# Kernel tuning notes

Hardware: AMD Instinct MI355X
Metric: run time of the kernel (lower is better)

Reference implementation:

```python
import jax, jax.numpy as jnp
import numpy as np

D = 512
HEADS, DIM_HEAD, LANDMARKS, PINV_ITERS = 8, 64, 256, 6
CONV_K = 33  # residual depthwise conv kernel over sequence dim


def _ln(x, g, b, eps=1e-5):
    mu = x.mean(-1, keepdims=True)
    var = ((x - mu) ** 2).mean(-1, keepdims=True)
    return (x - mu) / jnp.sqrt(var + eps) * g + b


def _moe(x, gw, gb, f1w, f1b, l1g, l1b, f2w, f2b, l2g, l2b, k):
    # Dense grouped-expert evaluation (same math as per-token dispatch in torch source).
    scores = x @ gw + gb                               # [B,N,E]
    topk_s, topk_i = jax.lax.top_k(scores, k)          # [B,N,k]
    h = jnp.einsum('bnd,edh->benh', x, f1w) + f1b[None, :, None, :]
    h = jax.nn.relu(_ln(h, l1g[None, :, None, :], l1b[None, :, None, :]))
    o = jnp.einsum('benh,ehd->bend', h, f2w) + f2b[None, :, None, :]
    o = _ln(o, l2g[None, :, None, :], l2b[None, :, None, :])  # [B,E,N,D]
    o = jnp.take_along_axis(jnp.swapaxes(o, 1, 2), topk_i[..., None], axis=2)  # [B,N,k,D]
    w = jax.nn.softmax(topk_s, axis=-1)[..., None]
    return (w * o).sum(axis=2) + x


def _pinv(x, iters):
    # Moore-Penrose iterative pseudoinverse (lucidrains nystrom-attention)
    col = jnp.abs(x).sum(-1).max()
    row = jnp.abs(x).sum(-2).max()
    z = jnp.swapaxes(x, -1, -2) / (col * row)
    I = jnp.eye(x.shape[-1], dtype=x.dtype)
    for _ in range(iters):
        xz = x @ z
        z = 0.25 * z @ (13 * I - xz @ (15 * I - xz @ (7 * I - xz)))
    return z


def _nystrom(x, qkv_w, out_w, out_b, conv_w):
    b, n, _ = x.shape
    m, h, dh = LANDMARKS, HEADS, DIM_HEAD
    pad = (m - n % m) % m
    x = jnp.pad(x, ((0, 0), (pad, 0), (0, 0)))  # pad at FRONT, as in source
    npd = n + pad
    qkv = x @ qkv_w                              # [b, npd, 3*h*dh]
    q, k, v = [t.reshape(b, npd, h, dh).transpose(0, 2, 1, 3) for t in jnp.split(qkv, 3, axis=-1)]
    q = q * dh ** -0.5
    l = npd // m
    q_l = q.reshape(b, h, m, l, dh).mean(3)      # landmark means
    k_l = k.reshape(b, h, m, l, dh).mean(3)
    attn1 = jax.nn.softmax(jnp.einsum('bhid,bhjd->bhij', q, k_l), -1)    # [b,h,npd,m]
    attn2 = jax.nn.softmax(jnp.einsum('bhid,bhjd->bhij', q_l, k_l), -1)  # [b,h,m,m]
    attn3 = jax.nn.softmax(jnp.einsum('bhid,bhjd->bhij', q_l, k), -1)    # [b,h,m,npd]
    out = (attn1 @ _pinv(attn2, PINV_ITERS)) @ (attn3 @ v)               # [b,h,npd,dh]
    res = jax.lax.conv_general_dilated(
        v, conv_w, (1, 1), [(CONV_K // 2, CONV_K // 2), (0, 0)],
        dimension_numbers=('NCHW', 'OIHW', 'NCHW'), feature_group_count=h)
    out = out + res
    out = out.transpose(0, 2, 1, 3).reshape(b, npd, h * dh)
    out = out @ out_w + out_b
    return out[:, -n:]


def setup_inputs() -> dict:
    key = jax.random.key(0)
    ks = iter(jax.random.split(key, 64))
    def rn(shape, s=0.02):
        return jax.random.normal(next(ks), shape, jnp.float32) * s
    inp = {'features': jax.random.normal(next(ks), (4, 6000, D), jnp.float32)}
    inp['cls_token'] = rn((1, 1, D), 1e-6)
    def moe_params(pfx, E):
        inp[pfx + '_gate_w'] = rn((D, E)); inp[pfx + '_gate_b'] = jnp.zeros((E,), jnp.float32)
        inp[pfx + '_fc1_w'] = rn((E, D, D)); inp[pfx + '_fc1_b'] = jnp.zeros((E, D), jnp.float32)
        inp[pfx + '_ln1_g'] = jnp.ones((E, D), jnp.float32); inp[pfx + '_ln1_b'] = jnp.zeros((E, D), jnp.float32)
        inp[pfx + '_fc2_w'] = rn((E, D, D)); inp[pfx + '_fc2_b'] = jnp.zeros((E, D), jnp.float32)
        inp[pfx + '_ln2_g'] = jnp.ones((E, D), jnp.float32); inp[pfx + '_ln2_b'] = jnp.zeros((E, D), jnp.float32)
    moe_params('moe1', 2)
    moe_params('moe2', 4)
    def layer_params(pfx):
        inp[pfx + '_norm_g'] = jnp.ones((D,), jnp.float32); inp[pfx + '_norm_b'] = jnp.zeros((D,), jnp.float32)
        inp[pfx + '_qkv_w'] = rn((D, 3 * HEADS * DIM_HEAD))
        inp[pfx + '_out_w'] = rn((HEADS * DIM_HEAD, D)); inp[pfx + '_out_b'] = jnp.zeros((D,), jnp.float32)
        inp[pfx + '_conv_w'] = rn((HEADS, 1, CONV_K, 1))
    layer_params('l1')
    layer_params('l2')
    return inp


def reference(features, cls_token,
              moe1_gate_w, moe1_gate_b, moe1_fc1_w, moe1_fc1_b, moe1_ln1_g, moe1_ln1_b, moe1_fc2_w, moe1_fc2_b, moe1_ln2_g, moe1_ln2_b,
              moe2_gate_w, moe2_gate_b, moe2_fc1_w, moe2_fc1_b, moe2_ln1_g, moe2_ln1_b, moe2_fc2_w, moe2_fc2_b, moe2_ln2_g, moe2_ln2_b,
              l1_norm_g, l1_norm_b, l1_qkv_w, l1_out_w, l1_out_b, l1_conv_w,
              l2_norm_g, l2_norm_b, l2_qkv_w, l2_out_w, l2_out_b, l2_conv_w):
    B, N, _ = features.shape
    _H = int(np.ceil(np.sqrt(N)))
    add = _H * _H - N
    h = jnp.concatenate([features, features[:, :add]], axis=1)      # square pad by wrap
    h = jnp.concatenate([jnp.broadcast_to(cls_token, (B, 1, D)), h], axis=1)
    h = _moe(h, moe1_gate_w, moe1_gate_b, moe1_fc1_w, moe1_fc1_b, moe1_ln1_g, moe1_ln1_b, moe1_fc2_w, moe1_fc2_b, moe1_ln2_g, moe1_ln2_b, k=1)
    h = h + _nystrom(_ln(h, l1_norm_g, l1_norm_b), l1_qkv_w, l1_out_w, l1_out_b, l1_conv_w)
    h = _moe(h, moe2_gate_w, moe2_gate_b, moe2_fc1_w, moe2_fc1_b, moe2_ln1_g, moe2_ln1_b, moe2_fc2_w, moe2_fc2_b, moe2_ln2_g, moe2_ln2_b, k=2)
    h = h + _nystrom(_ln(h, l2_norm_g, l2_norm_b), l2_qkv_w, l2_out_w, l2_out_b, l2_conv_w)
    return (h[:, 0], h[:, 1:])
```

## Files before the change

kernel.cpp:

```cpp
#include <hip/hip_runtime.h>
#include <hip/hip_bf16.h>

constexpr int BATCH = 4;
constexpr int NTOK  = 6085;
constexpr int BN_TOK = BATCH * NTOK;
constexpr int NPD   = 6144;
constexpr int RPAD  = BATCH * NPD;
constexpr int DMODEL = 512;
constexpr int NH = 8, DH = 64;
constexpr int NBH = BATCH * NH;
constexpr int LGRP = NPD / 256;
constexpr int PAD_FRONT = 59;
constexpr int CONVK = 33;
constexpr int NCH = 8;

typedef __attribute__((ext_vector_type(8))) short short8v;
typedef __attribute__((ext_vector_type(4))) float f32x4;

__device__ __forceinline__ unsigned short f2bf(float f) {
  unsigned u = __float_as_uint(f);
  u += 0x7FFF + ((u >> 16) & 1);
  return (unsigned short)(u >> 16);
}
__device__ __forceinline__ float bf2f(unsigned short h) {
  return __uint_as_float((unsigned)h << 16);
}


__global__ void k_build_h(const float* __restrict__ feat, const float* __restrict__ cls,
                          float* __restrict__ H) {
  size_t total = (size_t)BN_TOK * DMODEL;
  for (size_t idx = (size_t)blockIdx.x * blockDim.x + threadIdx.x; idx < total;
       idx += (size_t)gridDim.x * blockDim.x) {
    int d = (int)(idx & 511);
    size_t tok = idx >> 9;
    int b = (int)(tok / NTOK), n = (int)(tok % NTOK);
    float v;
    if (n == 0) v = cls[d];
    else {
      int i = n - 1; if (i >= 6000) i -= 6000;
      v = feat[((size_t)b * 6000 + i) * DMODEL + d];
    }
    H[idx] = v;
  }
}

__global__ void k_diag_fill(float* __restrict__ out, size_t n, float val) {
  for (size_t i = (size_t)blockIdx.x * blockDim.x + threadIdx.x; i < n;
       i += (size_t)gridDim.x * blockDim.x)
    out[i] = val;
}

__global__ __launch_bounds__(256) void k_wconv(const float* __restrict__ W, int ldb,
    unsigned short* __restrict__ hi, unsigned short* __restrict__ lo) {
  __shared__ unsigned short Th[64][80], Tl[64][80];
  int bk = blockIdx.y * 64, bn = blockIdx.x * 64;
  int t = threadIdx.x;
  int kr = t >> 2, cq = (t & 3) * 16;
  const float* src = W + (size_t)(bk + kr) * ldb + bn + cq;
  #pragma unroll
  for (int q = 0; q < 4; ++q) {
    float4 v = *(const float4*)(src + q * 4);
    float vs[4] = {v.x, v.y, v.z, v.w};
    #pragma unroll
    for (int e = 0; e < 4; ++e) {
      int n = cq + q * 4 + e;
      unsigned short h = f2bf(vs[e]);
      Th[n][kr] = h;
      Tl[n][kr] = f2bf(vs[e] - bf2f(h));
    }
  }
  __syncthreads();
  int nr = t >> 2, kq = (t & 3) * 16;
  size_t o = (size_t)(bn + nr) * 512 + bk + kq;
  *(short8v*)&hi[o]     = *(const short8v*)&Th[nr][kq];
  *(short8v*)&hi[o + 8] = *(const short8v*)&Th[nr][kq + 8];
  *(short8v*)&lo[o]     = *(const short8v*)&Tl[nr][kq];
  *(short8v*)&lo[o + 8] = *(const short8v*)&Tl[nr][kq + 8];
}

__global__ __launch_bounds__(256) void k_gemm_mfma(const float* __restrict__ A,
    const unsigned short* __restrict__ BtH, const unsigned short* __restrict__ BtL,
    const float* __restrict__ bias, float* __restrict__ C,
    int M, int lda, int ldc, float alpha, int omode, unsigned short* __restrict__ Clo)
{
  __shared__ unsigned short AsH[128][40], AsL[128][40];
  __shared__ unsigned short BsH[128][40], BsL[128][40];
  int bm = blockIdx.y * 128, bn = blockIdx.x * 128;
  int tid = threadIdx.x;
  int wave = tid >> 6, lane = tid & 63;
  int mo = (wave >> 1) * 64, no = (wave & 1) * 64;
  int r16 = lane & 15, g = lane >> 4;
  f32x4 acc[4][4] = {};
  int srow = tid >> 1, shalf = (tid & 1) * 16;
  const float* aptr = A + (size_t)(bm + srow) * lda + shalf;
  bool avalid = (bm + srow) < M;
  const unsigned short* bhptr = BtH + (size_t)(bn + srow) * 512 + shalf;
  const unsigned short* blptr = BtL + (size_t)(bn + srow) * 512 + shalf;
  for (int k0 = 0; k0 < 512; k0 += 32) {
    unsigned short h8[16], l8[16];
    #pragma unroll
    for (int q = 0; q < 4; ++q) {
      float4 v = avalid ? *(const float4*)(aptr + k0 + q * 4) : make_float4(0.f, 0.f, 0.f, 0.f);
      float vs[4] = {v.x, v.y, v.z, v.w};
      #pragma unroll
      for (int e = 0; e < 4; ++e) {
        unsigned short hh = f2bf(vs[e]);
        h8[q * 4 + e] = hh;
        l8[q * 4 + e] = f2bf(vs[e] - bf2f(hh));
      }
    }
    *(short8v*)&AsH[srow][shalf]     = *(short8v*)&h8[0];
    *(short8v*)&AsH[srow][shalf + 8] = *(short8v*)&h8[8];
    *(short8v*)&AsL[srow][shalf]     = *(short8v*)&l8[0];
    *(short8v*)&AsL[srow][shalf + 8] = *(short8v*)&l8[8];
    *(short8v*)&BsH[srow][shalf]     = *(const short8v*)(bhptr + k0);
    *(short8v*)&BsH[srow][shalf + 8] = *(const short8v*)(bhptr + k0 + 8);
    *(short8v*)&BsL[srow][shalf]     = *(const short8v*)(blptr + k0);
    *(short8v*)&BsL[srow][shalf + 8] = *(const short8v*)(blptr + k0 + 8);
    __syncthreads();
    short8v ah[4], al[4], bh[4], bl[4];
    #pragma unroll
    for (int mt = 0; mt < 4; ++mt) {
      ah[mt] = *(const short8v*)&AsH[mo + mt * 16 + r16][g * 8];
      al[mt] = *(const short8v*)&AsL[mo + mt * 16 + r16][g * 8];
    }
    #pragma unroll
    for (int nt = 0; nt < 4; ++nt) {
      bh[nt] = *(const short8v*)&BsH[no + nt * 16 + r16][g * 8];
      bl[nt] = *(const short8v*)&BsL[no + nt * 16 + r16][g * 8];
    }
    #pragma unroll
    for (int mt = 0; mt < 4; ++mt)
      #pragma unroll
      for (int nt = 0; nt < 4; ++nt) {
        acc[mt][nt] = __builtin_amdgcn_mfma_f32_16x16x32_bf16(ah[mt], bh[nt], acc[mt][nt], 0, 0, 0);
        acc[mt][nt] = __builtin_amdgcn_mfma_f32_16x16x32_bf16(ah[mt], bl[nt], acc[mt][nt], 0, 0, 0);
        acc[mt][nt] = __builtin_amdgcn_mfma_f32_16x16x32_bf16(al[mt], bh[nt], acc[mt][nt], 0, 0, 0);
      }
    __syncthreads();
  }
  #pragma unroll
  for (int mt = 0; mt < 4; ++mt)
    #pragma unroll
    for (int nt = 0; nt < 4; ++nt)
      #pragma unroll
      for (int j = 0; j < 4; ++j) {
        int gr = bm + mo + mt * 16 + g * 4 + j;
        int gc = bn + no + nt * 16 + r16;
        if (gr >= M) continue;
        float v = alpha * acc[mt][nt][j] + (bias ? bias[gc] : 0.f);
        if (omode == 0) {
          C[(size_t)gr * ldc + gc] = v;
        } else if (omode == 2) {
          int bb = gr / NPD, ii = gr % NPD;
          if (ii >= PAD_FRONT)
            C[((size_t)bb * NTOK + ii - PAD_FRONT) * 512 + gc] += v;
        } else if (omode == 3) {
          int bb = gr / NPD, ii = gr % NPD;
          int hh = gc >> 6, dd = gc & 63;
          C[(((size_t)bb * NH + hh) * NPD + ii) * 64 + dd] = v;
        } else {
          int bb = gr / NPD, ii = gr % NPD;
          int hh = gc >> 6, dd = gc & 63;
          size_t idx = (((size_t)bb * NH + hh) * NPD + ii) * 64 + dd;
          unsigned short hi = f2bf(v);
          ((unsigned short*)C)[idx] = hi;
          Clo[idx] = f2bf(v - bf2f(hi));
        }
      }
}

__global__ __launch_bounds__(256) void k_gemm_mfma2(const float* __restrict__ A,
    const float* __restrict__ Bt, float* __restrict__ C,
    float alpha, int omode, float cdiag, int premap)
{
  __shared__ unsigned short AsH[128][40], AsL[128][40];
  __shared__ unsigned short BsH[128][40], BsL[128][40];
  size_t zo = (size_t)blockIdx.z * 65536;
  int bm = blockIdx.y * 128, bn = blockIdx.x * 128;
  int tid = threadIdx.x;
  int wave = tid >> 6, lane = tid & 63;
  int mo = (wave >> 1) * 64, no = (wave & 1) * 64;
  int r16 = lane & 15, g = lane >> 4;
  f32x4 acc[4][4] = {};
  int srow = tid >> 1, shalf = (tid & 1) * 16;
  int grow = bm + srow;
  int gn = bn + srow;
  for (int k0 = 0; k0 < 256; k0 += 32) {
    unsigned short h8[16], l8[16];
    #pragma unroll
    for (int q = 0; q < 4; ++q) {
      float4 v = *(const float4*)&A[zo + (size_t)grow * 256 + k0 + shalf + q * 4];
      float vs[4] = {v.x, v.y, v.z, v.w};
      #pragma unroll
      for (int e = 0; e < 4; ++e) {
        float a = vs[e];
        if (premap) a = ((grow == (k0 + shalf + q * 4 + e)) ? 7.f : 0.f) - a;
        unsigned short hh = f2bf(a);
        h8[q * 4 + e] = hh;
        l8[q * 4 + e] = f2bf(a - bf2f(hh));
      }
    }
    *(short8v*)&AsH[srow][shalf]     = *(short8v*)&h8[0];
    *(short8v*)&AsH[srow][shalf + 8] = *(short8v*)&h8[8];
    *(short8v*)&AsL[srow][shalf]     = *(short8v*)&l8[0];
    *(short8v*)&AsL[srow][shalf + 8] = *(short8v*)&l8[8];
    #pragma unroll
    for (int q = 0; q < 4; ++q) {
      float4 v = *(const float4*)&Bt[zo + (size_t)gn * 256 + k0 + shalf + q * 4];
      float vs[4] = {v.x, v.y, v.z, v.w};
      #pragma unroll
      for (int e = 0; e < 4; ++e) {
        unsigned short hh = f2bf(vs[e]);
        h8[q * 4 + e] = hh;
        l8[q * 4 + e] = f2bf(vs[e] - bf2f(hh));
      }
    }
    *(short8v*)&BsH[srow][shalf]     = *(short8v*)&h8[0];
    *(short8v*)&BsH[srow][shalf + 8] = *(short8v*)&h8[8];
    *(short8v*)&BsL[srow][shalf]     = *(short8v*)&l8[0];
    *(short8v*)&BsL[srow][shalf + 8] = *(short8v*)&l8[8];
    __syncthreads();
    short8v ah[4], al[4], bh[4], bl[4];
    #pragma unroll
    for (int mt = 0; mt < 4; ++mt) {
      ah[mt] = *(const short8v*)&AsH[mo + mt * 16 + r16][g * 8];
      al[mt] = *(const short8v*)&AsL[mo + mt * 16 + r16][g * 8];
    }
    #pragma unroll
    for (int nt = 0; nt < 4; ++nt) {
      bh[nt] = *(const short8v*)&BsH[no + nt * 16 + r16][g * 8];
      bl[nt] = *(const short8v*)&BsL[no + nt * 16 + r16][g * 8];
    }
    #pragma unroll
    for (int mt = 0; mt < 4; ++mt)
      #pragma unroll
      for (int nt = 0; nt < 4; ++nt) {
        acc[mt][nt] = __builtin_amdgcn_mfma_f32_16x16x32_bf16(ah[mt], bh[nt], acc[mt][nt], 0, 0, 0);
        acc[mt][nt] = __builtin_amdgcn_mfma_f32_16x16x32_bf16(ah[mt], bl[nt], acc[mt][nt], 0, 0, 0);
        acc[mt][nt] = __builtin_amdgcn_mfma_f32_16x16x32_bf16(al[mt], bh[nt], acc[mt][nt], 0, 0, 0);
      }
    __syncthreads();
  }
  #pragma unroll
  for (int mt = 0; mt < 4; ++mt)
    #pragma unroll
    for (int nt = 0; nt < 4; ++nt)
      #pragma unroll
      for (int j = 0; j < 4; ++j) {
        int gr = bm + mo + mt * 16 + g * 4 + j;
        int gc = bn + no + nt * 16 + r16;
        float v;
        if (omode == 5) v = ((gr == gc) ? cdiag : 0.f) - acc[mt][nt][j];
        else            v = alpha * acc[mt][nt][j];
        C[zo + (size_t)gr * 256 + gc] = v;
      }
}

__global__ __launch_bounds__(256) void k_tpose(const float* __restrict__ in,
                                               float* __restrict__ out) {
  __shared__ float Ts[64][65];
  int bx = blockIdx.x * 64, by = blockIdx.y * 64;
  size_t zo = (size_t)blockIdx.z * 65536;
  int t = threadIdx.x;
  int r = t >> 4, c4 = (t & 15) * 4;
  #pragma unroll
  for (int u = 0; u < 4; ++u) {
    float4 v = *(const float4*)&in[zo + (size_t)(by + r + u * 16) * 256 + bx + c4];
    Ts[r + u * 16][c4 + 0] = v.x; Ts[r + u * 16][c4 + 1] = v.y;
    Ts[r + u * 16][c4 + 2] = v.z; Ts[r + u * 16][c4 + 3] = v.w;
  }
  __syncthreads();
  #pragma unroll
// ... 90 lines not shown
__global__ void k_gate(const float* __restrict__ X, const float* __restrict__ gw,
                       const float* __restrict__ gb, float* __restrict__ WT, int E, int k) {
  int tok = blockIdx.x; int lane = threadIdx.x;
  const float* x = X + (size_t)tok * DMODEL;
  float s[4] = {0.f, 0.f, 0.f, 0.f};
  for (int d = lane; d < DMODEL; d += 64) {
    float xv = x[d];
    for (int e = 0; e < E; ++e) s[e] += xv * gw[(size_t)d * E + e];
  }
  #pragma unroll
  for (int off = 32; off; off >>= 1) {
    #pragma unroll
    for (int e = 0; e < 4; ++e) s[e] += __shfl_down(s[e], off);
  }
  if (lane == 0) {
    for (int e = 0; e < E; ++e) s[e] += gb[e];
    float w[4] = {0.f, 0.f, 0.f, 0.f};
    int i1 = 0;
    for (int e = 1; e < E; ++e) if (s[e] > s[i1]) i1 = e;
    if (k == 1) {
      w[i1] = 1.f;
    } else {
      int i2 = -1;
      for (int e = 0; e < E; ++e) { if (e == i1) continue; if (i2 < 0 || s[e] > s[i2]) i2 = e; }
      float e2 = expf(s[i2] - s[i1]);
      float zz = 1.f + e2;
      w[i1] = 1.f / zz; w[i2] = e2 / zz;
    }
    #pragma unroll
    for (int e = 0; e < 4; ++e) WT[(size_t)tok * 4 + e] = w[e];
  }
}

__device__ __forceinline__ void wave_ln_stats(const float* x, int lane, float& mu, float& rstd) {
  float s = 0.f, q = 0.f;
  #pragma unroll
  for (int j = 0; j < 8; ++j) { float v = x[lane + 64 * j]; s += v; q += v * v; }
  #pragma unroll
  for (int off = 32; off; off >>= 1) { s += __shfl_xor(s, off); q += __shfl_xor(q, off); }
  mu = s * (1.f / 512.f);
  float var = q * (1.f / 512.f) - mu * mu;
  rstd = rsqrtf(var + 1e-5f);
}

__global__ void k_ln_relu(float* __restrict__ T, const float* __restrict__ g,
                          const float* __restrict__ b) {
  int row = blockIdx.x; int lane = threadIdx.x;
  float* x = T + (size_t)row * 512;
  float mu, rstd; wave_ln_stats(x, lane, mu, rstd);
  #pragma unroll
  for (int j = 0; j < 8; ++j) {
    int d = lane + 64 * j;
    float v = (x[d] - mu) * rstd * g[d] + b[d];
    x[d] = fmaxf(v, 0.f);
  }
}

__global__ void k_ln_waccum(const float* __restrict__ T, float* __restrict__ H,
                            const float* __restrict__ g, const float* __restrict__ b,
                            const float* __restrict__ WT, int e) {
  int row = blockIdx.x;
  float w = WT[(size_t)row * 4 + e];
  if (w == 0.f) return;
  int lane = threadIdx.x;
  const float* x = T + (size_t)row * 512;
  float mu, rstd; wave_ln_stats(x, lane, mu, rstd);
  float* h = H + (size_t)row * 512;
  #pragma unroll
  for (int j = 0; j < 8; ++j) {
    int d = lane + 64 * j;
    h[d] += w * ((x[d] - mu) * rstd * g[d] + b[d]);
  }
}

__global__ void k_ln_pad(const float* __restrict__ H, float* __restrict__ XLn,
                         const float* __restrict__ g, const float* __restrict__ b) {
  int row = blockIdx.x; int lane = threadIdx.x;
  int bb = row / NPD, i = row % NPD;
  float* y = XLn + (size_t)row * 512;
  if (i < PAD_FRONT) {
    #pragma unroll
    for (int j = 0; j < 8; ++j) y[lane + 64 * j] = 0.f;
    return;
  }
  const float* x = H + ((size_t)bb * NTOK + (i - PAD_FRONT)) * 512;
  float mu, rstd; wave_ln_stats(x, lane, mu, rstd);
  #pragma unroll
  for (int j = 0; j < 8; ++j) {
    int d = lane + 64 * j;
    y[d] = (x[d] - mu) * rstd * g[d] + b[d];
  }
}

__global__ void k_xmean(const float* __restrict__ XLn, float* __restrict__ Xm) {
  int z = blockIdx.x;
  int c = threadIdx.x;
  int b = z >> 8, jm = z & 255;
  const float* base = XLn + ((size_t)b * NPD + jm * LGRP) * 512 + c;
  float s = 0.f;
  #pragma unroll
  for (int t = 0; t < LGRP; ++t) s += base[(size_t)t * 512];
  Xm[(size_t)z * 512 + c] = s * (1.f / LGRP);
}

__global__ __launch_bounds__(256) void k_attn2(const float* __restrict__ QL,
                                               const float* __restrict__ KL,
                                               float* __restrict__ A2) {
  int z = blockIdx.x; int bh = z >> 8, j = z & 255;
  int b = bh >> 3, h = bh & 7;
  int t = threadIdx.x;
  __shared__ float q[64]; __shared__ float red[256];
  __shared__ float mshare, sshare;
  if (t < 64) q[t] = QL[((size_t)b * 256 + j) * 512 + h * 64 + t];
  __syncthreads();
  const float* kl = KL + ((size_t)b * 256 + t) * 512 + h * 64;
  float s = 0.f;
  #pragma unroll
  for (int d = 0; d < 64; ++d) s += q[d] * kl[d];
  red[t] = s; __syncthreads();
  for (int st = 128; st; st >>= 1) { if (t < st) red[t] = fmaxf(red[t], red[t + st]); __syncthreads(); }
  if (t == 0) mshare = red[0];
  __syncthreads();
  float e = expf(s - mshare);
  red[t] = e; __syncthreads();
  for (int st = 128; st; st >>= 1) { if (t < st) red[t] += red[t + st]; __syncthreads(); }
  if (t == 0) sshare = red[0];
  __syncthreads();
  A2[((size_t)bh * 256 + j) * 256 + t] = e / sshare;
}

__global__ __launch_bounds__(256) void k_pinv_scalars(const float* __restrict__ A2,
                                                      unsigned int* __restrict__ sc) {
  int bh = blockIdx.x; int t = threadIdx.x;
  const float* A = A2 + (size_t)bh * 65536;
// ... 134 lines not shown
    #pragma unroll
    for (int kk = 0; kk < 2; ++kk)
      #pragma unroll
      for (int nt = 0; nt < 4; ++nt) {
        short8v kh = *(const short8v*)&KsH[nt * 16 + r16][kk * 32 + g * 8];
        short8v kl = *(const short8v*)&KsL[nt * 16 + r16][kk * 32 + g * 8];
        S[nt] = __builtin_amdgcn_mfma_f32_16x16x32_bf16(qh[kk], kh, S[nt], 0, 0, 0);
        S[nt] = __builtin_amdgcn_mfma_f32_16x16x32_bf16(qh[kk], kl, S[nt], 0, 0, 0);
        S[nt] = __builtin_amdgcn_mfma_f32_16x16x32_bf16(ql[kk], kh, S[nt], 0, 0, 0);
      }
    float tmax[4];
    #pragma unroll
    for (int j = 0; j < 4; ++j)
      tmax[j] = fmaxf(fmaxf(S[0][j], S[1][j]), fmaxf(S[2][j], S[3][j]));
    #pragma unroll
    for (int off = 8; off; off >>= 1)
      #pragma unroll
      for (int j = 0; j < 4; ++j) tmax[j] = fmaxf(tmax[j], __shfl_xor(tmax[j], off));
    float corr[4];
    #pragma unroll
    for (int j = 0; j < 4; ++j) {
      float mn = fmaxf(m[j], tmax[j]);
      corr[j] = expf(m[j] - mn);
      m[j] = mn;
    }
    __syncthreads();
    float tl[4] = {0.f, 0.f, 0.f, 0.f};
    #pragma unroll
    for (int nt = 0; nt < 4; ++nt)
      #pragma unroll
      for (int j = 0; j < 4; ++j) {
        float p = expf(S[nt][j] - m[j]);
        tl[j] += p;
        unsigned short ph = f2bf(p);
        KsH[wave * 16 + g * 4 + j][nt * 16 + r16] = ph;
        KsL[wave * 16 + g * 4 + j][nt * 16 + r16] = f2bf(p - bf2f(ph));
      }
    #pragma unroll
    for (int off = 8; off; off >>= 1)
      #pragma unroll
      for (int j = 0; j < 4; ++j) tl[j] += __shfl_xor(tl[j], off);
    #pragma unroll
    for (int j = 0; j < 4; ++j) lsum[j] = lsum[j] * corr[j] + tl[j];
    #pragma unroll
    for (int nt = 0; nt < 4; ++nt)
      #pragma unroll
      for (int j = 0; j < 4; ++j) O4[nt][j] *= corr[j];
    #pragma unroll
    for (int kk = 0; kk < 2; ++kk) {
      short8v ph = *(const short8v*)&KsH[wave * 16 + r16][kk * 32 + g * 8];
      short8v pl = *(const short8v*)&KsL[wave * 16 + r16][kk * 32 + g * 8];
      #pragma unroll
      for (int nt = 0; nt < 4; ++nt) {
        short8v vh = *(const short8v*)&VtH[nt * 16 + r16][kk * 32 + g * 8];
        short8v vl = *(const short8v*)&VtL[nt * 16 + r16][kk * 32 + g * 8];
        O4[nt] = __builtin_amdgcn_mfma_f32_16x16x32_bf16(ph, vh, O4[nt], 0, 0, 0);
        O4[nt] = __builtin_amdgcn_mfma_f32_16x16x32_bf16(ph, vl, O4[nt], 0, 0, 0);
        O4[nt] = __builtin_amdgcn_mfma_f32_16x16x32_bf16(pl, vh, O4[nt], 0, 0, 0);
      }
    }
  }
  if (mode == 0) {
    float* Ob = Op + (size_t)b * Osb + (size_t)h * Osh;
    float inv[4];
    #pragma unroll
    for (int j = 0; j < 4; ++j) inv[j] = 1.f / lsum[j];
    #pragma unroll
    for (int nt = 0; nt < 4; ++nt)
      #pragma unroll
      for (int j = 0; j < 4; ++j)
        Ob[(size_t)(q0 + g * 4 + j) * Osr + nt * 16 + r16] = O4[nt][j] * inv[j];
  } else {
    #pragma unroll
    for (int j = 0; j < 4; ++j) {
      size_t rowbase = ((size_t)ch * NBH + bh) * 256 + q0 + g * 4 + j;
      #pragma unroll
      for (int nt = 0; nt < 4; ++nt)
        Opart[rowbase * 64 + nt * 16 + r16] = O4[nt][j];
      if (r16 == 0) { ML[rowbase * 2] = m[j]; ML[rowbase * 2 + 1] = lsum[j]; }
    }
  }
}

__global__ __launch_bounds__(256) void k_flash_comb(const float* __restrict__ Opart,
                                                    const float* __restrict__ ML,
                                                    float* __restrict__ A3V) {
  int jt = blockIdx.x, bh = blockIdx.y;
  int t = threadIdx.x;
  int jr = t >> 4, q16 = t & 15;
  int row = jt * 16 + jr;
  float mv[NCH], lv[NCH];
// ... 101 lines not shown
  constexpr size_t SZ_ROW  = (size_t)RPAD * 512;
  float* W = (float*)d_ws;
  float* H  = W;
  float* WT = W + SZ_H;
  unsigned int* SC = (unsigned int*)(W + SZ_H + 97360);
  float* pool = W + SZ_H + 97360 + 16;

  float* R2 = pool;
  float* R3 = pool + SZ_ROW;
  float* R4 = pool + 2 * SZ_ROW;
  float* SMALL = pool + 3 * SZ_ROW;
  float* Xm  = SMALL;
  float* QL  = SMALL + 524288;
  float* KL  = SMALL + 1048576;
  float* A2  = SMALL + 1572864;
  float* Zb  = SMALL + 3670016;
  float* XZp = SMALL + 5767168;
  float* Wa  = SMALL + 7864320;
  float* Wb  = SMALL + 9961472;
  float* A3V = SMALL + 12058624;
  float* W2b = SMALL + 12582912;
  size_t total_f = (SZ_H + 97360 + 16) + 3 * SZ_ROW + 13107200;
  if (total_f * 4 > ws_size) {
    k_diag_fill<<<2048, 256, 0, stream>>>((float*)d_out, (size_t)out_size,
                                          (float)(ws_size >> 20));
    return;
  }

  k_build_h<<<2048, 256, 0, stream>>>(feat, cls, H);

  auto run_moe = [&](const float* gw, const float* gb, const float* f1w, const float* f1b,
                     const float* l1g, const float* l1b, const float* f2w, const float* f2b,
                     const float* l2g, const float* l2b, int E, int k) {
    float* T1 = R2; float* T2 = R3; float* Xsnap = R4;
    unsigned short* BtHi = (unsigned short*)A2;
    unsigned short* BtLo = (unsigned short*)(A2 + 131072);
    hipMemcpyAsync(Xsnap, H, SZ_H * 4, hipMemcpyDeviceToDevice, stream);
    k_gate<<<BN_TOK, 64, 0, stream>>>(H, gw, gb, WT, E, k);
    dim3 g(4, (BN_TOK + 127) / 128, 1);
    for (int e = 0; e < E; ++e) {
      k_wconv<<<dim3(8, 8), 256, 0, stream>>>(f1w + (size_t)e * 262144, 512, BtHi, BtLo);
      k_gemm_mfma<<<g, 256, 0, stream>>>(Xsnap, BtHi, BtLo, f1b + e * 512, T1,
          BN_TOK, 512, 512, 1.f, 0, nullptr);
      k_ln_relu<<<BN_TOK, 64, 0, stream>>>(T1, l1g + e * 512, l1b + e * 512);
      k_wconv<<<dim3(8, 8), 256, 0, stream>>>(f2w + (size_t)e * 262144, 512, BtHi, BtLo);
      k_gemm_mfma<<<g, 256, 0, stream>>>(T1, BtHi, BtLo, f2b + e * 512, T2,
          BN_TOK, 512, 512, 1.f, 0, nullptr);
      k_ln_waccum<<<BN_TOK, 64, 0, stream>>>(T2, H, l2g + e * 512, l2b + e * 512, WT, e);
    }
  };

  auto run_attn = [&](const float* ng, const float* nb, const float* qkvw, const float* outw,
                      const float* outb, const float* convw) {
    float* XLn = R2; float* AttnO = R2;
    float* Qb = R3;
    unsigned short* VrH = (unsigned short*)R3;
    unsigned short* VrL = VrH + 12582912;
    unsigned short* KH  = (unsigned short*)R3;
    unsigned short* KLo = KH + 12582912;
    unsigned short* VtH = (unsigned short*)R4;
    unsigned short* VtL = VtH + 12582912;
    k_ln_pad<<<RPAD, 64, 0, stream>>>(H, XLn, ng, nb);
    k_xmean<<<BATCH * 256, 512, 0, stream>>>(XLn, Xm);
    k_gemm<<<dim3(8, 16, 1), 256, 0, stream>>>(Xm, qkvw, nullptr, QL,
        1024, 512, 512, 512, 1536, 512, 0, 0, 0, 0.125f, 0, 0.f);
    k_gemm<<<dim3(8, 16, 1), 256, 0, stream>>>(Xm, qkvw + 512, nullptr, KL,
        1024, 512, 512, 512, 1536, 512, 0, 0, 0, 1.f, 0, 0.f);
    k_attn2<<<NBH * 256, 256, 0, stream>>>(QL, KL, A2);
    hipMemsetAsync(SC, 0, 8, stream);
    k_pinv_scalars<<<NBH, 256, 0, stream>>>(A2, SC);
    k_y0<<<2048, 256, 0, stream>>>(A2, Zb, SC);
    k_zinit<<<2048, 256, 0, stream>>>(A2, Wb, SC);
    float* Y = Zb; float* Z = Wb; float* F1 = XZp; float* F2 = Wa;
    dim3 gq(2, 2, NBH);
    for (int it = 0; it < 6; ++it) {
      k_gemm_mfma2<<<gq, 256, 0, stream>>>(A2, Y, F1, 1.f, 0, 0.f, 0);
      k_tpose<<<dim3(4, 4, NBH), 256, 0, stream>>>(F1, F2);
      k_gemm_mfma2<<<gq, 256, 0, stream>>>(F2, F1, Y, 1.f, 5, 15.f, 1);
      k_gemm_mfma2<<<gq, 256, 0, stream>>>(Y, F1, F2, 1.f, 5, 13.f, 0);
      k_gemm_mfma2<<<gq, 256, 0, stream>>>(Z, F2, F1, 0.25f, 0, 0.f, 0);
      float* tz = Z; Z = F1; F1 = tz;
      if (it < 5)
        k_tpose<<<dim3(4, 4, NBH), 256, 0, stream>>>(Z, Y);
    }
    unsigned short* KLH = (unsigned short*)A2;
    unsigned short* KLL = KLH + 524288;
    unsigned short* W2tH = KLH + 1048576;
    unsigned short* W2tL = KLH + 1572864;
    k_cvt_kl<<<2048, 256, 0, stream>>>(KL, KLH, KLL);
    unsigned short* BtQH = (unsigned short*)Wa;
    unsigned short* BtQL = BtQH + 786432;
    k_wconv<<<dim3(24, 8), 256, 0, stream>>>(qkvw, 1536, BtQH, BtQL);
    dim3 gr(4, (RPAD + 127) / 128, 1);
    k_gemm_mfma<<<gr, 256, 0, stream>>>(XLn, BtQH + 1024 * 512, BtQL + 1024 * 512, nullptr,
        (float*)VrH, RPAD, 512, 512, 1.f, 6, VrL);
    k_vtpose<<<dim3(NPD / 64, NBH), 256, 0, stream>>>(VrH, VrL, VtH, VtL);
    k_gemm_mfma<<<gr, 256, 0, stream>>>(XLn, BtQH + 512 * 512, BtQL + 512 * 512, nullptr,
        (float*)KH, RPAD, 512, 512, 1.f, 6, KLo);
    k_flash_pre<<<dim3(4, NBH, NCH), 256, 0, stream>>>(
        QL, 131072LL, 64LL, 512,
        KH, KLo, (long long)NPD * 64,
        VtH, VtL, (long long)64 * NPD, NPD,
        nullptr, 0, 0, 0, Zb, Xm, NPD / (64 * NCH), 1);
    k_flash_comb<<<dim3(16, NBH), 256, 0, stream>>>(Zb, Xm, A3V);
    k_gemm<<<dim3(1, 4, NBH), 256, 0, stream>>>(Z, A3V, nullptr, W2b,
        256, 64, 256, 256, 64, 64, 65536, 16384, 16384, 1.f, 0, 0.f);
    k_cvt_w2t<<<2048, 256, 0, stream>>>(W2b, W2tH, W2tL);
    k_gemm_mfma<<<gr, 256, 0, stream>>>(XLn, BtQH, BtQL, nullptr,
        Qb, RPAD, 512, 512, 0.125f, 0, nullptr);
    k_flash_pre<<<dim3(NPD / 64, NBH, 1), 256, 0, stream>>>(
        Qb, (long long)NPD * 512, 64LL, 512,
        KLH, KLL, 16384LL,
        W2tH, W2tL, 16384LL, 256,
        AttnO, (long long)NPD * 512, 64LL, 512,
        nullptr, nullptr, 4, 0);
    k_conv_add<<<dim3(NPD / 128, NBH), 256, 0, stream>>>(VtH, VtL, convw, AttnO);
    unsigned short* BtOH = (unsigned short*)Wa;
    unsigned short* BtOL = BtOH + 262144;
    k_wconv<<<dim3(8, 8), 256, 0, stream>>>(outw, 512, BtOH, BtOL);
    k_gemm_mfma<<<gr, 256, 0, stream>>>(AttnO, BtOH, BtOL, outb,
        H, RPAD, 512, 512, 1.f, 2, nullptr);
  };

  run_moe(m1_gw, m1_gb, m1_f1w, m1_f1b, m1_l1g, m1_l1b, m1_f2w, m1_f2b, m1_l2g, m1_l2b, 2, 1);
  run_attn(l1_ng, l1_nb, l1_qkvw, l1_outw, l1_outb, l1_convw);
  run_moe(m2_gw, m2_gb, m2_f1w, m2_f1b, m2_l1g, m2_l1b, m2_f2w, m2_f2b, m2_l2g, m2_l2b, 4, 2);
  run_attn(l2_ng, l2_nb, l2_qkvw, l2_outw, l2_outb, l2_convw);

  k_out_write<<<2048, 256, 0, stream>>>(H, (float*)d_out);
}
```

Baseline: 3.611 ms.

## Pre-split activations into bf16 hi/lo and reduce precision in pinv and flash

```diff
diff --git a/kernel.cpp b/kernel.cpp
--- a/kernel.cpp
+++ b/kernel.cpp
@@ -51,6 +51,19 @@
     out[i] = val;
 }
 
+__global__ void k_split(const float* __restrict__ src, unsigned short* __restrict__ dst) {
+  int row = blockIdx.x; int lane = threadIdx.x;
+  const float* x = src + (size_t)row * 512;
+  unsigned short* p = dst + (size_t)row * 1024;
+  #pragma unroll
+  for (int j = 0; j < 8; ++j) {
+    int d = lane + 64 * j;
+    float v = x[d];
+    unsigned short h = f2bf(v);
+    p[d] = h; p[512 + d] = f2bf(v - bf2f(h));
+  }
+}
+
 __global__ __launch_bounds__(256) void k_wconv(const float* __restrict__ W, int ldb,
     unsigned short* __restrict__ hi, unsigned short* __restrict__ lo) {
   __shared__ unsigned short Th[64][80], Tl[64][80];
@@ -79,10 +92,10 @@
   *(short8v*)&lo[o + 8] = *(const short8v*)&Tl[nr][kq + 8];
 }
 
-__global__ __launch_bounds__(256) void k_gemm_mfma(const float* __restrict__ A,
+__global__ __launch_bounds__(256) void k_gemm_pre(const unsigned short* __restrict__ AHL,
     const unsigned short* __restrict__ BtH, const unsigned short* __restrict__ BtL,
     const float* __restrict__ bias, float* __restrict__ C,
-    int M, int lda, int ldc, float alpha, int omode, unsigned short* __restrict__ Clo)
+    int M, int ldc, float alpha, int omode, unsigned short* __restrict__ Clo)
 {
   __shared__ unsigned short AsH[128][40], AsL[128][40];
   __shared__ unsigned short BsH[128][40], BsL[128][40];
@@ -93,27 +106,21 @@
   int r16 = lane & 15, g = lane >> 4;
   f32x4 acc[4][4] = {};
   int srow = tid >> 1, shalf = (tid & 1) * 16;
-  const float* aptr = A + (size_t)(bm + srow) * lda + shalf;
+  const unsigned short* aptr = AHL + (size_t)(bm + srow) * 1024;
   bool avalid = (bm + srow) < M;
   const unsigned short* bhptr = BtH + (size_t)(bn + srow) * 512 + shalf;
   const unsigned short* blptr = BtL + (size_t)(bn + srow) * 512 + shalf;
+  short8v zero8 = {0,0,0,0,0,0,0,0};
   for (int k0 = 0; k0 < 512; k0 += 32) {
-    unsigned short h8[16], l8[16];
-    #pragma unroll
-    for (int q = 0; q < 4; ++q) {
-      float4 v = avalid ? *(const float4*)(aptr + k0 + q * 4) : make_float4(0.f, 0.f, 0.f, 0.f);
-      float vs[4] = {v.x, v.y, v.z, v.w};
-      #pragma unroll
-      for (int e = 0; e < 4; ++e) {
-        unsigned short hh = f2bf(vs[e]);
-        h8[q * 4 + e] = hh;
-        l8[q * 4 + e] = f2bf(vs[e] - bf2f(hh));
-      }
-    }
-    *(short8v*)&AsH[srow][shalf]     = *(short8v*)&h8[0];
-    *(short8v*)&AsH[srow][shalf + 8] = *(short8v*)&h8[8];
-    *(short8v*)&AsL[srow][shalf]     = *(short8v*)&l8[0];
-    *(short8v*)&AsL[srow][shalf + 8] = *(short8v*)&l8[8];
+    if (avalid) {
+      *(short8v*)&AsH[srow][shalf]     = *(const short8v*)(aptr + k0 + shalf);
+      *(short8v*)&AsH[srow][shalf + 8] = *(const short8v*)(aptr + k0 + shalf + 8);
+      *(short8v*)&AsL[srow][shalf]     = *(const short8v*)(aptr + 512 + k0 + shalf);
+      *(short8v*)&AsL[srow][shalf + 8] = *(const short8v*)(aptr + 512 + k0 + shalf + 8);
+    } else {
+      *(short8v*)&AsH[srow][shalf] = zero8; *(short8v*)&AsH[srow][shalf + 8] = zero8;
+      *(short8v*)&AsL[srow][shalf] = zero8; *(short8v*)&AsL[srow][shalf + 8] = zero8;
+    }
     *(short8v*)&BsH[srow][shalf]     = *(const short8v*)(bhptr + k0);
     *(short8v*)&BsH[srow][shalf + 8] = *(const short8v*)(bhptr + k0 + 8);
     *(short8v*)&BsL[srow][shalf]     = *(const short8v*)(blptr + k0);
@@ -171,9 +178,90 @@
       }
 }
 
+__global__ __launch_bounds__(256) void k_gemm_mfma(const float* __restrict__ A,
+    const unsigned short* __restrict__ BtH, const unsigned short* __restrict__ BtL,
+    const float* __restrict__ bias, float* __restrict__ C,
+    int M, int lda, int ldc, float alpha, int omode)
+{
+  __shared__ unsigned short AsH[128][40], AsL[128][40];
+  __shared__ unsigned short BsH[128][40], BsL[128][40];
+  int bm = blockIdx.y * 128, bn = blockIdx.x * 128;
+  int tid = threadIdx.x;
+  int wave = tid >> 6, lane = tid & 63;
+  int mo = (wave >> 1) * 64, no = (wave & 1) * 64;
+  int r16 = lane & 15, g = lane >> 4;
+  f32x4 acc[4][4] = {};
+  int srow = tid >> 1, shalf = (tid & 1) * 16;
+  const float* aptr = A + (size_t)(bm + srow) * lda + shalf;
+  bool avalid = (bm + srow) < M;
+  const unsigned short* bhptr = BtH + (size_t)(bn + srow) * 512 + shalf;
+  const unsigned short* blptr = BtL + (size_t)(bn + srow) * 512 + shalf;
+  for (int k0 = 0; k0 < 512; k0 += 32) {
+    unsigned short h8[16], l8[16];
+    #pragma unroll
+    for (int q = 0; q < 4; ++q) {
+      float4 v = avalid ? *(const float4*)(aptr + k0 + q * 4) : make_float4(0.f, 0.f, 0.f, 0.f);
+      float vs[4] = {v.x, v.y, v.z, v.w};
+      #pragma unroll
+      for (int e = 0; e < 4; ++e) {
+        unsigned short hh = f2bf(vs[e]);
+        h8[q * 4 + e] = hh;
+        l8[q * 4 + e] = f2bf(vs[e] - bf2f(hh));
+      }
+    }
+    *(short8v*)&AsH[srow][shalf]     = *(short8v*)&h8[0];
+    *(short8v*)&AsH[srow][shalf + 8] = *(short8v*)&h8[8];
+    *(short8v*)&AsL[srow][shalf]     = *(short8v*)&l8[0];
+    *(short8v*)&AsL[srow][shalf + 8] = *(short8v*)&l8[8];
+    *(short8v*)&BsH[srow][shalf]     = *(const short8v*)(bhptr + k0);
+    *(short8v*)&BsH[srow][shalf + 8] = *(const short8v*)(bhptr + k0 + 8);
+    *(short8v*)&BsL[srow][shalf]     = *(const short8v*)(blptr + k0);
+    *(short8v*)&BsL[srow][shalf + 8] = *(const short8v*)(blptr + k0 + 8);
+    __syncthreads();
+    short8v ah[4], al[4], bh[4], bl[4];
+    #pragma unroll
+    for (int mt = 0; mt < 4; ++mt) {
+      ah[mt] = *(const short8v*)&AsH[mo + mt * 16 + r16][g * 8];
+      al[mt] = *(const short8v*)&AsL[mo + mt * 16 + r16][g * 8];
+    }
+    #pragma unroll
+    for (int nt = 0; nt < 4; ++nt) {
+      bh[nt] = *(const short8v*)&BsH[no + nt * 16 + r16][g * 8];
+      bl[nt] = *(const short8v*)&BsL[no + nt * 16 + r16][g * 8];
+    }
+    #pragma unroll
+    for (int mt = 0; mt < 4; ++mt)
+      #pragma unroll
+      for (int nt = 0; nt < 4; ++nt) {
+        acc[mt][nt] = __builtin_amdgcn_mfma_f32_16x16x32_bf16(ah[mt], bh[nt], acc[mt][nt], 0, 0, 0);
+        acc[mt][nt] = __builtin_amdgcn_mfma_f32_16x16x32_bf16(ah[mt], bl[nt], acc[mt][nt], 0, 0, 0);
+        acc[mt][nt] = __builtin_amdgcn_mfma_f32_16x16x32_bf16(al[mt], bh[nt], acc[mt][nt], 0, 0, 0);
+      }
+    __syncthreads();
+  }
+  #pragma unroll
+  for (int mt = 0; mt < 4; ++mt)
+    #pragma unroll
+    for (int nt = 0; nt < 4; ++nt)
+      #pragma unroll
+      for (int j = 0; j < 4; ++j) {
+        int gr = bm + mo + mt * 16 + g * 4 + j;
+        int gc = bn + no + nt * 16 + r16;
+        if (gr >= M) continue;
+        float v = alpha * acc[mt][nt][j] + (bias ? bias[gc] : 0.f);
+        if (omode == 0) {
+          C[(size_t)gr * ldc + gc] = v;
+        } else if (omode == 2) {
+          int bb = gr / NPD, ii = gr % NPD;
+          if (ii >= PAD_FRONT)
+            C[((size_t)bb * NTOK + ii - PAD_FRONT) * 512 + gc] += v;
+        }
+      }
+}
+
 __global__ __launch_bounds__(256) void k_gemm_mfma2(const float* __restrict__ A,
     const float* __restrict__ Bt, float* __restrict__ C,
-    float alpha, int omode, float cdiag, int premap)
+    float alpha, int omode, float cdiag, int premap, int nprod)
 {
   __shared__ unsigned short AsH[128][40], AsL[128][40];
   __shared__ unsigned short BsH[128][40], BsL[128][40];
@@ -199,7 +287,7 @@
         if (premap) a = ((grow == (k0 + shalf + q * 4 + e)) ? 7.f : 0.f) - a;
         unsigned short hh = f2bf(a);
         h8[q * 4 + e] = hh;
-        l8[q * 4 + e] = f2bf(a - bf2f(hh));
+        l8[q * 4 + e] = (nprod == 3) ? f2bf(a - bf2f(hh)) : (unsigned short)0;
       }
     }
     *(short8v*)&AsH[srow][shalf]     = *(short8v*)&h8[0];
@@ -214,7 +302,7 @@
       for (int e = 0; e < 4; ++e) {
         unsigned short hh = f2bf(vs[e]);
         h8[q * 4 + e] = hh;
-        l8[q * 4 + e] = f2bf(vs[e] - bf2f(hh));
+        l8[q * 4 + e] = (nprod == 3) ? f2bf(vs[e] - bf2f(hh)) : (unsigned short)0;
       }
     }
     *(short8v*)&BsH[srow][shalf]     = *(short8v*)&h8[0];
@@ -238,8 +326,10 @@
       #pragma unroll
       for (int nt = 0; nt < 4; ++nt) {
         acc[mt][nt] = __builtin_amdgcn_mfma_f32_16x16x32_bf16(ah[mt], bh[nt], acc[mt][nt], 0, 0, 0);
-        acc[mt][nt] = __builtin_amdgcn_mfma_f32_16x16x32_bf16(ah[mt], bl[nt], acc[mt][nt], 0, 0, 0);
-        acc[mt][nt] = __builtin_amdgcn_mfma_f32_16x16x32_bf16(al[mt], bh[nt], acc[mt][nt], 0, 0, 0);
+        if (nprod == 3) {
+          acc[mt][nt] = __builtin_amdgcn_mfma_f32_16x16x32_bf16(ah[mt], bl[nt], acc[mt][nt], 0, 0, 0);
+          acc[mt][nt] = __builtin_amdgcn_mfma_f32_16x16x32_bf16(al[mt], bh[nt], acc[mt][nt], 0, 0, 0);
+        }
       }
     __syncthreads();
   }
@@ -396,10 +486,10 @@
   }
 }
 
-__device__ __forceinline__ void wave_ln_stats(const float* x, int lane, float& mu, float& rstd) {
+__device__ __forceinline__ void stats_from(const float* vals, float& mu, float& rstd) {
   float s = 0.f, q = 0.f;
   #pragma unroll
-  for (int j = 0; j < 8; ++j) { float v = x[lane + 64 * j]; s += v; q += v * v; }
+  for (int j = 0; j < 8; ++j) { s += vals[j]; q += vals[j] * vals[j]; }
   #pragma unroll
   for (int off = 32; off; off >>= 1) { s += __shfl_xor(s, off); q += __shfl_xor(q, off); }
   mu = s * (1.f / 512.f);
@@ -407,16 +497,22 @@
   rstd = rsqrtf(var + 1e-5f);
 }
 
-__global__ void k_ln_relu(float* __restrict__ T, const float* __restrict__ g,
-                          const float* __restrict__ b) {
+__global__ void k_ln_relu_split(float* __restrict__ T, const float* __restrict__ g,
+                                const float* __restrict__ b) {
   int row = blockIdx.x; int lane = threadIdx.x;
   float* x = T + (size_t)row * 512;
-  float mu, rstd; wave_ln_stats(x, lane, mu, rstd);
+  float vals[8];
+  #pragma unroll
+  for (int j = 0; j < 8; ++j) vals[j] = x[lane + 64 * j];
+  float mu, rstd; stats_from(vals, mu, rstd);
+  __syncthreads();
+  unsigned short* p = (unsigned short*)x;
   #pragma unroll
   for (int j = 0; j < 8; ++j) {
     int d = lane + 64 * j;
-    float v = (x[d] - mu) * rstd * g[d] + b[d];
-    x[d] = fmaxf(v, 0.f);
+    float v = fmaxf((vals[j] - mu) * rstd * g[d] + b[d], 0.f);
+    unsigned short h = f2bf(v);
+    p[d] = h; p[512 + d] = f2bf(v - bf2f(h));
   }
 }
 
@@ -428,42 +524,53 @@
   if (w == 0.f) return;
   int lane = threadIdx.x;
   const float* x = T + (size_t)row * 512;
-  float mu, rstd; wave_ln_stats(x, lane, mu, rstd);
+  float vals[8];
+  #pragma unroll
+  for (int j = 0; j < 8; ++j) vals[j] = x[lane + 64 * j];
+  float mu, rstd; stats_from(vals, mu, rstd);
   float* h = H + (size_t)row * 512;
   #pragma unroll
   for (int j = 0; j < 8; ++j) {
     int d = lane + 64 * j;
-    h[d] += w * ((x[d] - mu) * rstd * g[d] + b[d]);
-  }
-}
-
-__global__ void k_ln_pad(const float* __restrict__ H, float* __restrict__ XLn,
-                         const float* __restrict__ g, const float* __restrict__ b) {
+    h[d] += w * ((vals[j] - mu) * rstd * g[d] + b[d]);
+  }
+}
+
+__global__ void k_ln_pad_split(const float* __restrict__ H, unsigned short* __restrict__ XLn,
+                               const float* __restrict__ g, const float* __restrict__ b) {
   int row = blockIdx.x; int lane = threadIdx.x;
   int bb = row / NPD, i = row % NPD;
-  float* y = XLn + (size_t)row * 512;
+  unsigned short* y = XLn + (size_t)row * 1024;
   if (i < PAD_FRONT) {
     #pragma unroll
-    for (int j = 0; j < 8; ++j) y[lane + 64 * j] = 0.f;
+    for (int j = 0; j < 8; ++j) { y[lane + 64 * j] = 0; y[512 + lane + 64 * j] = 0; }
     return;
   }
   const float* x = H + ((size_t)bb * NTOK + (i - PAD_FRONT)) * 512;
-  float mu, rstd; wave_ln_stats(x, lane, mu, rstd);
+  float vals[8];
+  #pragma unroll
+  for (int j = 0; j < 8; ++j) vals[j] = x[lane + 64 * j];
+  float mu, rstd; stats_from(vals, mu, rstd);
   #pragma unroll
   for (int j = 0; j < 8; ++j) {
     int d = lane + 64 * j;
-    y[d] = (x[d] - mu) * rstd * g[d] + b[d];
-  }
-}
-
-__global__ void k_xmean(const float* __restrict__ XLn, float* __restrict__ Xm) {
+    float v = (vals[j] - mu) * rstd * g[d] + b[d];
+    unsigned short h = f2bf(v);
+    y[d] = h; y[512 + d] = f2bf(v - bf2f(h));
+  }
+}
+
+__global__ void k_xmean_hl(const unsigned short* __restrict__ XLn, float* __restrict__ Xm) {
   int z = blockIdx.x;
   int c = threadIdx.x;
   int b = z >> 8, jm = z & 255;
-  const float* base = XLn + ((size_t)b * NPD + jm * LGRP) * 512 + c;
+  const unsigned short* base = XLn + ((size_t)b * NPD + jm * LGRP) * 1024;
   float s = 0.f;
   #pragma unroll
-  for (int t = 0; t < LGRP; ++t) s += base[(size_t)t * 512];
+  for (int t = 0; t < LGRP; ++t) {
+    const unsigned short* p = base + (size_t)t * 1024;
+    s += bf2f(p[c]) + bf2f(p[512 + c]);
+  }
   Xm[(size_t)z * 512 + c] = s * (1.f / LGRP);
 }
 
@@ -664,9 +771,7 @@
       for (int j = 0; j < 4; ++j) {
         float p = expf(S[nt][j] - m[j]);
         tl[j] += p;
-        unsigned short ph = f2bf(p);
-        KsH[wave * 16 + g * 4 + j][nt * 16 + r16] = ph;
-        KsL[wave * 16 + g * 4 + j][nt * 16 + r16] = f2bf(p - bf2f(ph));
+        KsH[wave * 16 + g * 4 + j][nt * 16 + r16] = f2bf(p);
       }
     #pragma unroll
     for (int off = 8; off; off >>= 1)
@@ -681,14 +786,12 @@
     #pragma unroll
     for (int kk = 0; kk < 2; ++kk) {
       short8v ph = *(const short8v*)&KsH[wave * 16 + r16][kk * 32 + g * 8];
-      short8v pl = *(const short8v*)&KsL[wave * 16 + r16][kk * 32 + g * 8];
       #pragma unroll
       for (int nt = 0; nt < 4; ++nt) {
         short8v vh = *(const short8v*)&VtH[nt * 16 + r16][kk * 32 + g * 8];
         short8v vl = *(const short8v*)&VtL[nt * 16 + r16][kk * 32 + g * 8];
         O4[nt] = __builtin_amdgcn_mfma_f32_16x16x32_bf16(ph, vh, O4[nt], 0, 0, 0);
         O4[nt] = __builtin_amdgcn_mfma_f32_16x16x32_bf16(ph, vl, O4[nt], 0, 0, 0);
-        O4[nt] = __builtin_amdgcn_mfma_f32_16x16x32_bf16(pl, vh, O4[nt], 0, 0, 0);
       }
     }
   }
@@ -856,27 +959,30 @@
   auto run_moe = [&](const float* gw, const float* gb, const float* f1w, const float* f1b,
                      const float* l1g, const float* l1b, const float* f2w, const float* f2b,
                      const float* l2g, const float* l2b, int E, int k) {
-    float* T1 = R2; float* T2 = R3; float* Xsnap = R4;
+    float* T1 = R2; float* T2 = R3;
+    unsigned short* XsHL = (unsigned short*)R4;
+    unsigned short* T1HL = (unsigned short*)R2;
     unsigned short* BtHi = (unsigned short*)A2;
     unsigned short* BtLo = (unsigned short*)(A2 + 131072);
-    hipMemcpyAsync(Xsnap, H, SZ_H * 4, hipMemcpyDeviceToDevice, stream);
+    k_split<<<BN_TOK, 64, 0, stream>>>(H, XsHL);
     k_gate<<<BN_TOK, 64, 0, stream>>>(H, gw, gb, WT, E, k);
     dim3 g(4, (BN_TOK + 127) / 128, 1);
     for (int e = 0; e < E; ++e) {
       k_wconv<<<dim3(8, 8), 256, 0, stream>>>(f1w + (size_t)e * 262144, 512, BtHi, BtLo);
-      k_gemm_mfma<<<g, 256, 0, stream>>>(Xsnap, BtHi, BtLo, f1b + e * 512, T1,
-          BN_TOK, 512, 512, 1.f, 0, nullptr);
-      k_ln_relu<<<BN_TOK, 64, 0, stream>>>(T1, l1g + e * 512, l1b + e * 512);
+      k_gemm_pre<<<g, 256, 0, stream>>>(XsHL, BtHi, BtLo, f1b + e * 512, T1,
+          BN_TOK, 512, 1.f, 0, nullptr);
+      k_ln_relu_split<<<BN_TOK, 64, 0, stream>>>(T1, l1g + e * 512, l1b + e * 512);
       k_wconv<<<dim3(8, 8), 256, 0, stream>>>(f2w + (size_t)e * 262144, 512, BtHi, BtLo);
-      k_gemm_mfma<<<g, 256, 0, stream>>>(T1, BtHi, BtLo, f2b + e * 512, T2,
-          BN_TOK, 512, 512, 1.f, 0, nullptr);
+      k_gemm_pre<<<g, 256, 0, stream>>>(T1HL, BtHi, BtLo, f2b + e * 512, T2,
+          BN_TOK, 512, 1.f, 0, nullptr);
       k_ln_waccum<<<BN_TOK, 64, 0, stream>>>(T2, H, l2g + e * 512, l2b + e * 512, WT, e);
     }
   };
 
   auto run_attn = [&](const float* ng, const float* nb, const float* qkvw, const float* outw,
                       const float* outb, const float* convw) {
-    float* XLn = R2; float* AttnO = R2;
+    unsigned short* XLnHL = (unsigned short*)R2;
+    float* AttnO = R2;
     float* Qb = R3;
     unsigned short* VrH = (unsigned short*)R3;
     unsigned short* VrL = VrH + 12582912;
@@ -884,8 +990,8 @@
     unsigned short* KLo = KH + 12582912;
     unsigned short* VtH = (unsigned short*)R4;
     unsigned short* VtL = VtH + 12582912;
-    k_ln_pad<<<RPAD, 64, 0, stream>>>(H, XLn, ng, nb);
-    k_xmean<<<BATCH * 256, 512, 0, stream>>>(XLn, Xm);
+    k_ln_pad_split<<<RPAD, 64, 0, stream>>>(H, XLnHL, ng, nb);
+    k_xmean_hl<<<BATCH * 256, 512, 0, stream>>>(XLnHL, Xm);
     k_gemm<<<dim3(8, 16, 1), 256, 0, stream>>>(Xm, qkvw, nullptr, QL,
         1024, 512, 512, 512, 1536, 512, 0, 0, 0, 0.125f, 0, 0.f);
     k_gemm<<<dim3(8, 16, 1), 256, 0, stream>>>(Xm, qkvw + 512, nullptr, KL,
@@ -898,11 +1004,12 @@
     float* Y = Zb; float* Z = Wb; float* F1 = XZp; float* F2 = Wa;
     dim3 gq(2, 2, NBH);
     for (int it = 0; it < 6; ++it) {
-      k_gemm_mfma2<<<gq, 256, 0, stream>>>(A2, Y, F1, 1.f, 0, 0.f, 0);
+      int np = (it < 4) ? 1 : 3;
+      k_gemm_mfma2<<<gq, 256, 0, stream>>>(A2, Y, F1, 1.f, 0, 0.f, 0, np);
       k_tpose<<<dim3(4, 4, NBH), 256, 0, stream>>>(F1, F2);
-      k_gemm_mfma2<<<gq, 256, 0, stream>>>(F2, F1, Y, 1.f, 5, 15.f, 1);
-      k_gemm_mfma2<<<gq, 256, 0, stream>>>(Y, F1, F2, 1.f, 5, 13.f, 0);
-      k_gemm_mfma2<<<gq, 256, 0, stream>>>(Z, F2, F1, 0.25f, 0, 0.f, 0);
+      k_gemm_mfma2<<<gq, 256, 0, stream>>>(F2, F1, Y, 1.f, 5, 15.f, 1, np);
+      k_gemm_mfma2<<<gq, 256, 0, stream>>>(Y, F1, F2, 1.f, 5, 13.f, 0, np);
+      k_gemm_mfma2<<<gq, 256, 0, stream>>>(Z, F2, F1, 0.25f, 0, 0.f, 0, np);
       float* tz = Z; Z = F1; F1 = tz;
       if (it < 5)
         k_tpose<<<dim3(4, 4, NBH), 256, 0, stream>>>(Z, Y);
@@ -916,11 +1023,11 @@
     unsigned short* BtQL = BtQH + 786432;
     k_wconv<<<dim3(24, 8), 256, 0, stream>>>(qkvw, 1536, BtQH, BtQL);
     dim3 gr(4, (RPAD + 127) / 128, 1);
-    k_gemm_mfma<<<gr, 256, 0, stream>>>(XLn, BtQH + 1024 * 512, BtQL + 1024 * 512, nullptr,
-        (float*)VrH, RPAD, 512, 512, 1.f, 6, VrL);
+    k_gemm_pre<<<gr, 256, 0, stream>>>(XLnHL, BtQH + 1024 * 512, BtQL + 1024 * 512, nullptr,
+        (float*)VrH, RPAD, 512, 1.f, 6, VrL);
     k_vtpose<<<dim3(NPD / 64, NBH), 256, 0, stream>>>(VrH, VrL, VtH, VtL);
-    k_gemm_mfma<<<gr, 256, 0, stream>>>(XLn, BtQH + 512 * 512, BtQL + 512 * 512, nullptr,
-        (float*)KH, RPAD, 512, 512, 1.f, 6, KLo);
+    k_gemm_pre<<<gr, 256, 0, stream>>>(XLnHL, BtQH + 512 * 512, BtQL + 512 * 512, nullptr,
+        (float*)KH, RPAD, 512, 1.f, 6, KLo);
     k_flash_pre<<<dim3(4, NBH, NCH), 256, 0, stream>>>(
         QL, 131072LL, 64LL, 512,
         KH, KLo, (long long)NPD * 64,
@@ -930,8 +1037,8 @@
     k_gemm<<<dim3(1, 4, NBH), 256, 0, stream>>>(Z, A3V, nullptr, W2b,
         256, 64, 256, 256, 64, 64, 65536, 16384, 16384, 1.f, 0, 0.f);
     k_cvt_w2t<<<2048, 256, 0, stream>>>(W2b, W2tH, W2tL);
-    k_gemm_mfma<<<gr, 256, 0, stream>>>(XLn, BtQH, BtQL, nullptr,
-        Qb, RPAD, 512, 512, 0.125f, 0, nullptr);
+    k_gemm_pre<<<gr, 256, 0, stream>>>(XLnHL, BtQH, BtQL, nullptr,
+        Qb, RPAD, 512, 0.125f, 0, nullptr);
     k_flash_pre<<<dim3(NPD / 64, NBH, 1), 256, 0, stream>>>(
         Qb, (long long)NPD * 512, 64LL, 512,
         KLH, KLL, 16384LL,
@@ -943,7 +1050,7 @@
     unsigned short* BtOL = BtOH + 262144;
     k_wconv<<<dim3(8, 8), 256, 0, stream>>>(outw, 512, BtOH, BtOL);
     k_gemm_mfma<<<gr, 256, 0, stream>>>(AttnO, BtOH, BtOL, outb,
-        H, RPAD, 512, 512, 1.f, 2, nullptr);
+        H, RPAD, 512, 512, 1.f, 2);
   };
 
   run_moe(m1_gw, m1_gb, m1_f1w, m1_f1b, m1_l1g, m1_l1b, m1_f2w, m1_f2b, m1_l2g, m1_l2b, 2, 1);
```

Measured after the change: 4.287 ms. +18.7%, slower.
